# Kernel optimization log

Measured on AMD Instinct MI355X. Metric: run time of the kernel, lower is better.

The kernel has to match this reference:

```python
import jax, jax.numpy as jnp
import numpy as np

NSLICES = 4
HID = 512
IN_FEAT = 342   # input_shape - 1 (last column is phase)
OUT = 311
BATCH = 256


def cubic(y0, y1, y2, y3, mu):
    # Catmull-Rom cubic interpolation, as in the original PFNN code
    return (
        (-0.5 * y0 + 1.5 * y1 - 1.5 * y2 + 0.5 * y3) * mu * mu * mu
        + (y0 - 2.5 * y1 + 2.0 * y2 - 0.5 * y3) * mu * mu
        + (-0.5 * y0 + 0.5 * y2) * mu
        + y1
    )


def setup_inputs() -> dict:
    key = jax.random.key(0)
    ks = jax.random.split(key, 7)
    x = jax.random.uniform(ks[0], (BATCH, IN_FEAT + 1), dtype=jnp.float32)
    s = 0.02
    W0 = jax.random.normal(ks[1], (NSLICES, HID, IN_FEAT), dtype=jnp.float32) * s
    b0 = jax.random.normal(ks[2], (NSLICES, HID), dtype=jnp.float32) * s
    W1 = jax.random.normal(ks[3], (NSLICES, HID, HID), dtype=jnp.float32) * s
    b1 = jax.random.normal(ks[4], (NSLICES, HID), dtype=jnp.float32) * s
    W2 = jax.random.normal(ks[5], (NSLICES, OUT, HID), dtype=jnp.float32) * s
    b2 = jax.random.normal(ks[6], (NSLICES, OUT), dtype=jnp.float32) * s
    return {"x": x, "W0": W0, "b0": b0, "W1": W1, "b1": b1, "W2": W2, "b2": b2}


def reference(x, W0, b0, W1, b1, W2, b2):
    phase = x[:, -1]                       # [B]
    pscale = NSLICES * phase
    mu = jnp.mod(pscale, 1.0)              # [B]
    i1 = jnp.floor(pscale).astype(jnp.int32) % NSLICES
    i0 = (i1 - 1) % NSLICES
    i2 = (i1 + 1) % NSLICES
    i3 = (i1 + 2) % NSLICES
    muW = mu[:, None, None]                # broadcast over (out, in)
    mub = mu[:, None]

    Wb0 = cubic(W0[i0], W0[i1], W0[i2], W0[i3], muW)   # [B, 512, 342]
    bb0 = cubic(b0[i0], b0[i1], b0[i2], b0[i3], mub)   # [B, 512]
    Wb1 = cubic(W1[i0], W1[i1], W1[i2], W1[i3], muW)   # [B, 512, 512]
    bb1 = cubic(b1[i0], b1[i1], b1[i2], b1[i3], mub)
    Wb2 = cubic(W2[i0], W2[i1], W2[i2], W2[i3], muW)   # [B, 311, 512]
    bb2 = cubic(b2[i0], b2[i1], b2[i2], b2[i3], mub)

    h = x[:, :-1]                                       # [B, 342]
    h = jax.nn.elu(jnp.einsum('boi,bi->bo', Wb0, h) + bb0)
    h = jax.nn.elu(jnp.einsum('boi,bi->bo', Wb1, h) + bb1)
    out = jnp.einsum('boi,bi->bo', Wb2, h) + bb2        # [B, 311]
    return out
```

## Files before the change

kernel.cpp:

```cpp
#include <hip/hip_runtime.h>
#include <math.h>

#define HID 512
#define IN_FEAT 342
#define OUTD 311
#define BATCH 256
#define XROW (IN_FEAT + 1)

#define NT1 32
#define NCC1 16
#define NT2 20
#define NCC2 16
#define NCC0 11

typedef unsigned short u16;
typedef short bf16x8 __attribute__((ext_vector_type(8)));
typedef float f32x4 __attribute__((ext_vector_type(4)));

__device__ __forceinline__ u16 f2bf_rne(float v) {
    unsigned int x = __float_as_uint(v);
    unsigned int r = (x + 0x7fffu + ((x >> 16) & 1u)) >> 16;
    return (u16)r;
}
__device__ __forceinline__ float bf2f(u16 u) {
    return __uint_as_float(((unsigned int)u) << 16);
}

union U8 { u16 u[8]; uint4 v; };

__device__ __forceinline__ void split8(const float* __restrict__ src, bf16x8& hi, bf16x8& lo) {
#pragma unroll
    for (int j = 0; j < 8; j++) {
        u16 h = f2bf_rne(src[j]);
        hi[j] = (short)h;
        lo[j] = (short)f2bf_rne(src[j] - bf2f(h));
    }
}

#define NB0 32
#define KLDS0 360
__global__ __launch_bounds__(512, 1) void layer0_fused(
    const float* __restrict__ W0, const float* __restrict__ W1, const float* __restrict__ W2,
    const float* __restrict__ x, const float* __restrict__ bias,
    u16* __restrict__ F1, u16* __restrict__ F2,
    float* __restrict__ Oact, float* __restrict__ H2acc, float* __restrict__ outz)
{
    __shared__ u16 wlds[4 * NCC0 * 1024];
    __shared__ u16 hlds[2 * NB0 * KLDS0];
    __shared__ float accs[4][NB0][17];

    const int blk = (int)blockIdx.x;
    const int bx = (blk >> 3) & 7;
    const int by = (blk & 7) | ((blk >> 6) << 3);
    const int tid = (int)threadIdx.x;
    const int b0 = bx * NB0;
    const int o0 = by * 16;

    for (int idx = tid; idx < 4 * 16 * 44; idx += 512) {
        int s = idx / (16 * 44);
        int rem = idx - s * (16 * 44);
        int rr = rem / 44, c = rem - rr * 44;
        int k = c * 8;
        const float* rp = W0 + (size_t)(s * 512 + o0 + rr) * IN_FEAT;
        float src[8];
        if (k + 8 <= IN_FEAT) {
            const float2* p2 = reinterpret_cast<const float2*>(rp + k);
            float2 v0 = p2[0], v1 = p2[1], v2 = p2[2], v3 = p2[3];
            src[0] = v0.x; src[1] = v0.y; src[2] = v1.x; src[3] = v1.y;
            src[4] = v2.x; src[5] = v2.y; src[6] = v3.x; src[7] = v3.y;
        } else {
#pragma unroll
            for (int j = 0; j < 8; j++) src[j] = (k + j < IN_FEAT) ? rp[k + j] : 0.f;
        }
        U8 hi, lo;
#pragma unroll
        for (int j = 0; j < 8; j++) {
            u16 h = f2bf_rne(src[j]);
            hi.u[j] = h;
            lo.u[j] = f2bf_rne(src[j] - bf2f(h));
        }
        int cc = c >> 2, lane = (c & 3) * 16 + rr;
        *reinterpret_cast<uint4*>(&wlds[(s * NCC0 + cc) * 1024 + lane * 8])       = hi.v;
        *reinterpret_cast<uint4*>(&wlds[(s * NCC0 + cc) * 1024 + 512 + lane * 8]) = lo.v;
    }

    for (int idx = tid; idx < NB0 * 44; idx += 512) {
        int r = idx / 44, c = idx - r * 44;
        int k = c * 8;
        const float* xr = x + (size_t)(b0 + r) * XROW;
        float src[8];
#pragma unroll
        for (int j = 0; j < 8; j++) {
            int kk = k + j;
            src[j] = (kk < IN_FEAT) ? xr[kk] : 0.f;
        }
        bf16x8 hi, lo;
        split8(src, hi, lo);
        *reinterpret_cast<bf16x8*>(&hlds[r * KLDS0 + k])               = hi;
        *reinterpret_cast<bf16x8*>(&hlds[NB0 * KLDS0 + r * KLDS0 + k]) = lo;
    }
    __syncthreads();

    const int lane = tid & 63;
    const int w = tid >> 6;
    const int s = w & 3;
    const int t = w >> 2;
    const int m = lane & 15;
    const int q = lane >> 4;

    const u16* wf  = &wlds[s * NCC0 * 1024 + lane * 8];
    const u16* hp  = &hlds[(t * 16 + m) * KLDS0 + q * 8];
    const u16* hpl = &hlds[NB0 * KLDS0 + (t * 16 + m) * KLDS0 + q * 8];

    const int brow = b0 + t * 16 + m;
    const float ps = 4.f * x[(size_t)brow * XROW + IN_FEAT];
    const float fl = floorf(ps);
    const float mu = ps - fl;
    const int i1 = ((int)fl) & 3;
    const int jj = (s - i1) & 3;
    const float mu2 = mu * mu, mu3 = mu2 * mu;
    const float ds = (jj == 0) ? ( 1.5f * mu3 - 2.5f * mu2 + 1.0f)
                   : (jj == 1) ? (-1.5f * mu3 + 2.0f * mu2 + 0.5f * mu)
                   : (jj == 2) ? ( 0.5f * mu3 - 0.5f * mu2)
                   :             (-0.5f * mu3 + mu2 - 0.5f * mu);

    f32x4 a0 = {0.f, 0.f, 0.f, 0.f};
    f32x4 a1 = {0.f, 0.f, 0.f, 0.f};
    f32x4 a2 = {0.f, 0.f, 0.f, 0.f};
#pragma unroll
    for (int cc = 0; cc < NCC0; ++cc) {
        bf16x8 ah = *reinterpret_cast<const bf16x8*>(wf + cc * 1024);
        bf16x8 al = *reinterpret_cast<const bf16x8*>(wf + cc * 1024 + 512);
        bf16x8 bh = *reinterpret_cast<const bf16x8*>(hp + cc * 32);
        bf16x8 bl = *reinterpret_cast<const bf16x8*>(hpl + cc * 32);
        a0 = __builtin_amdgcn_mfma_f32_16x16x32_bf16(ah, bh, a0, 0, 0, 0);
        a1 = __builtin_amdgcn_mfma_f32_16x16x32_bf16(ah, bl, a1, 0, 0, 0);
        a2 = __builtin_amdgcn_mfma_f32_16x16x32_bf16(al, bh, a2, 0, 0, 0);
    }
    __syncthreads();

    f32x4 sum = a0 + a1 + a2;
#pragma unroll
    for (int r = 0; r < 4; ++r) {
        int o = o0 + q * 4 + r;
        accs[s][t * 16 + m][q * 4 + r] = ds * (sum[r] + bias[(size_t)s * HID + o]);
    }
    __syncthreads();

    const int b_l = tid >> 4;
    const int o_l = tid & 15;
    float vv = accs[0][b_l][o_l] + accs[1][b_l][o_l]
             + accs[2][b_l][o_l] + accs[3][b_l][o_l];
    {
        float e = (vv > 0.f) ? vv : expm1f(vv);
        Oact[(size_t)(b0 + b_l) * HID + o0 + o_l] = e;
    }

    if (blk < 208) {
        const bool w2j = (blk >= 128);
        int l = w2j ? (blk - 128) : blk;
        int js, jot;
        if (w2j) { js = l / 20; jot = l - js * 20; }
        else     { js = l >> 5; jot = l & 31; }
        u16* Fd = w2j ? (F2 + (size_t)(js * NT2 + jot) * NCC2 * 1024)
                      : (F1 + (size_t)(js * NT1 + jot) * NCC1 * 1024);
        for (int idx = tid; idx < 16 * 64; idx += 512) {
            int rr = idx >> 6, c = idx & 63;
            float src[8] = {0.f, 0.f, 0.f, 0.f, 0.f, 0.f, 0.f, 0.f};
            if (!w2j) {
                const float4* p4 = reinterpret_cast<const float4*>(
                    W1 + (size_t)(js * 512 + jot * 16 + rr) * 512 + c * 8);
                float4 v0 = p4[0], v1 = p4[1];
                src[0] = v0.x; src[1] = v0.y; src[2] = v0.z; src[3] = v0.w;
                src[4] = v1.x; src[5] = v1.y; src[6] = v1.z; src[7] = v1.w;
            } else {
                int orow = jot * 16 + rr;
                if (orow < OUTD) {
                    const float4* p4 = reinterpret_cast<const float4*>(
                        W2 + ((size_t)js * OUTD + orow) * 512 + c * 8);
                    float4 v0 = p4[0], v1 = p4[1];
                    src[0] = v0.x; src[1] = v0.y; src[2] = v0.z; src[3] = v0.w;
                    src[4] = v1.x; src[5] = v1.y; src[6] = v1.z; src[7] = v1.w;
                }
            }
            U8 hi, lo;
#pragma unroll
            for (int j = 0; j < 8; j++) {
                u16 h = f2bf_rne(src[j]);
                hi.u[j] = h;
                lo.u[j] = f2bf_rne(src[j] - bf2f(h));
            }
            int cc = c >> 2, jl = (c & 3) * 16 + rr;
            *reinterpret_cast<uint4*>(Fd + cc * 1024 + jl * 8)       = hi.v;
            *reinterpret_cast<uint4*>(Fd + cc * 1024 + 512 + jl * 8) = lo.v;
        }
    } else {
        for (int i = (blk - 208) * 512 + tid; i < 131072 + 79616; i += 48 * 512) {
            if (i < 131072) H2acc[i] = 0.f;
            else            outz[i - 131072] = 0.f;
        }
    }
}

#define KLDS1 264
template<int FINAL, int ACT, int NT, int NBY>
__global__ __launch_bounds__(256, 4) void layer_ks(
    const u16* __restrict__ Wf, const float* __restrict__ x,
    const float* __restrict__ Hin, const float* __restrict__ bias, int Mb,
    float* __restrict__ accout)
{
    union SharedU {
        u16 h[2][16 * KLDS1];
        float acc[4][16][17];
    };
    __shared__ SharedU sm;

    const int blk = (int)blockIdx.x;
    const int bx = (blk >> 3) & 15;
    const int kh = (blk >> 7) & 1;
    const int by = (blk & 7) | ((blk >> 8) << 3);
    if (by >= NBY) return;

    const int tid = (int)threadIdx.x;
    const int b0 = bx * 16;
    const int o0 = by * 16;

    for (int idx = tid; idx < 16 * 32; idx += 256) {
        int r = idx >> 5, c = idx & 31;
        const float4* hv = reinterpret_cast<const float4*>(
            Hin + (size_t)(b0 + r) * HID + kh * 256 + c * 8);
        float4 v0 = hv[0], v1 = hv[1];
        float src[8] = {v0.x, v0.y, v0.z, v0.w, v1.x, v1.y, v1.z, v1.w};
        if (ACT) {
#pragma unroll
            for (int j = 0; j < 8; j++) src[j] = (src[j] > 0.f) ? src[j] : expm1f(src[j]);
        }
        bf16x8 hi, lo;
        split8(src, hi, lo);
        *reinterpret_cast<bf16x8*>(&sm.h[0][r * KLDS1 + c * 8]) = hi;
        *reinterpret_cast<bf16x8*>(&sm.h[1][r * KLDS1 + c * 8]) = lo;
    }
    __syncthreads();

    const int lane = tid & 63;
    const int s = tid >> 6;
    const int m = lane & 15;
    const int q = lane >> 4;

    const u16* wf = Wf + ((size_t)(s * NT + by) * 16 + kh * 8) * 1024 + lane * 8;
    const u16* hp  = &sm.h[0][m * KLDS1 + q * 8];
    const u16* hpl = &sm.h[1][m * KLDS1 + q * 8];

    const int brow = b0 + m;
    const float ps = 4.f * x[(size_t)brow * XROW + IN_FEAT];
    const float fl = floorf(ps);
    const float mu = ps - fl;
    const int i1 = ((int)fl) & 3;
    const int jj = (s - i1) & 3;
    const float mu2 = mu * mu, mu3 = mu2 * mu;
    const float ds = (jj == 0) ? ( 1.5f * mu3 - 2.5f * mu2 + 1.0f)
                   : (jj == 1) ? (-1.5f * mu3 + 2.0f * mu2 + 0.5f * mu)
                   : (jj == 2) ? ( 0.5f * mu3 - 0.5f * mu2)
                   :             (-0.5f * mu3 + mu2 - 0.5f * mu);

    f32x4 a0 = {0.f, 0.f, 0.f, 0.f};
    f32x4 a1 = {0.f, 0.f, 0.f, 0.f};
    f32x4 a2 = {0.f, 0.f, 0.f, 0.f};
#pragma unroll
    for (int cc = 0; cc < 8; ++cc) {
        bf16x8 ah = *reinterpret_cast<const bf16x8*>(wf + cc * 1024);
        bf16x8 al = *reinterpret_cast<const bf16x8*>(wf + cc * 1024 + 512);
        bf16x8 bh = *reinterpret_cast<const bf16x8*>(hp + cc * 32);
        bf16x8 bl = *reinterpret_cast<const bf16x8*>(hpl + cc * 32);
        a0 = __builtin_amdgcn_mfma_f32_16x16x32_bf16(ah, bh, a0, 0, 0, 0);
        a1 = __builtin_amdgcn_mfma_f32_16x16x32_bf16(ah, bl, a1, 0, 0, 0);
        a2 = __builtin_amdgcn_mfma_f32_16x16x32_bf16(al, bh, a2, 0, 0, 0);
    }
    __syncthreads();

    f32x4 sum = a0 + a1 + a2;
#pragma unroll
    for (int r = 0; r < 4; ++r) {
        int o = o0 + q * 4 + r;
        float bb = (kh == 0 && o < Mb) ? bias[(size_t)s * Mb + o] : 0.f;
        sm.acc[s][m][q * 4 + r] = ds * (sum[r] + bb);
    }
    __syncthreads();

    const int b_l = tid >> 4;
    const int o_l = tid & 15;
    float vv = sm.acc[0][b_l][o_l] + sm.acc[1][b_l][o_l]
             + sm.acc[2][b_l][o_l] + sm.acc[3][b_l][o_l];
    const int o = o0 + o_l;
    const int b = b0 + b_l;
    if (FINAL) {
        if (o < OUTD) unsafeAtomicAdd(&accout[(size_t)b * OUTD + o], vv);
    } else {
        unsafeAtomicAdd(&accout[(size_t)b * HID + o], vv);
    }
}

extern "C" void kernel_launch(void* const* d_in, const int* in_sizes, int n_in,
                              void* d_out, int out_size, void* d_ws, size_t ws_size,
                              hipStream_t stream) {
    const float* x  = (const float*)d_in[0];
    const float* W0 = (const float*)d_in[1];
    const float* b0v = (const float*)d_in[2];
    const float* W1 = (const float*)d_in[3];
    const float* b1v = (const float*)d_in[4];
    const float* W2 = (const float*)d_in[5];
    const float* b2v = (const float*)d_in[6];
    float* out = (float*)d_out;

    char* pw = (char*)d_ws;
    auto alloc = [&](size_t bytes) { char* r = pw; pw += (bytes + 255) & ~(size_t)255; return r; };

    u16* F1 = (u16*)alloc((size_t)4 * NT1 * NCC1 * 1024 * 2);
    u16* F2 = (u16*)alloc((size_t)4 * NT2 * NCC2 * 1024 * 2);
    float* H0act = (float*)alloc((size_t)BATCH * HID * 4);
    float* H2acc = (float*)alloc((size_t)BATCH * HID * 4);

    layer0_fused<<<256, 512, 0, stream>>>(
        W0, W1, W2, x, b0v, F1, F2, H0act, H2acc, out);

    layer_ks<0, 0, NT1, 32><<<1024, 256, 0, stream>>>(
        F1, x, H0act, b1v, HID, H2acc);

    layer_ks<1, 1, NT2, 20><<<768, 256, 0, stream>>>(
        F2, x, H2acc, b2v, OUTD, out);
}
```

Baseline: 99.99 us.

## Hoist global weight loads ahead of LDS staging to overlap memory latency

In the fused layer-0 kernel, the W1/W2 reformat job's global loads are now issued at kernel start into registers, before the W0/x staging and the MFMA work, and written out at the end. The staging loops are unrolled with fixed trip counts. In layer_ks, the first four weight fragments are prefetched from global before the activation staging barrier, and the K loop is software-pipelined to load the next fragments while the current ones feed the MFMAs. The aim is to hide global-load latency behind other work, at the cost of more live registers and possible occupancy pressure.

```diff
diff --git a/kernel.cpp b/kernel.cpp
--- a/kernel.cpp
+++ b/kernel.cpp
@@ -56,51 +56,6 @@
     const int b0 = bx * NB0;
     const int o0 = by * 16;
 
-    for (int idx = tid; idx < 4 * 16 * 44; idx += 512) {
-        int s = idx / (16 * 44);
-        int rem = idx - s * (16 * 44);
-        int rr = rem / 44, c = rem - rr * 44;
-        int k = c * 8;
-        const float* rp = W0 + (size_t)(s * 512 + o0 + rr) * IN_FEAT;
-        float src[8];
-        if (k + 8 <= IN_FEAT) {
-            const float2* p2 = reinterpret_cast<const float2*>(rp + k);
-            float2 v0 = p2[0], v1 = p2[1], v2 = p2[2], v3 = p2[3];
-            src[0] = v0.x; src[1] = v0.y; src[2] = v1.x; src[3] = v1.y;
-            src[4] = v2.x; src[5] = v2.y; src[6] = v3.x; src[7] = v3.y;
-        } else {
-#pragma unroll
-            for (int j = 0; j < 8; j++) src[j] = (k + j < IN_FEAT) ? rp[k + j] : 0.f;
-        }
-        U8 hi, lo;
-#pragma unroll
-        for (int j = 0; j < 8; j++) {
-            u16 h = f2bf_rne(src[j]);
-            hi.u[j] = h;
-            lo.u[j] = f2bf_rne(src[j] - bf2f(h));
-        }
-        int cc = c >> 2, lane = (c & 3) * 16 + rr;
-        *reinterpret_cast<uint4*>(&wlds[(s * NCC0 + cc) * 1024 + lane * 8])       = hi.v;
-        *reinterpret_cast<uint4*>(&wlds[(s * NCC0 + cc) * 1024 + 512 + lane * 8]) = lo.v;
-    }
-
-    for (int idx = tid; idx < NB0 * 44; idx += 512) {
-        int r = idx / 44, c = idx - r * 44;
-        int k = c * 8;
-        const float* xr = x + (size_t)(b0 + r) * XROW;
-        float src[8];
-#pragma unroll
-        for (int j = 0; j < 8; j++) {
-            int kk = k + j;
-            src[j] = (kk < IN_FEAT) ? xr[kk] : 0.f;
-        }
-        bf16x8 hi, lo;
-        split8(src, hi, lo);
-        *reinterpret_cast<bf16x8*>(&hlds[r * KLDS0 + k])               = hi;
-        *reinterpret_cast<bf16x8*>(&hlds[NB0 * KLDS0 + r * KLDS0 + k]) = lo;
-    }
-    __syncthreads();
-
     const int lane = tid & 63;
     const int w = tid >> 6;
     const int s = w & 3;
@@ -108,15 +63,107 @@
     const int m = lane & 15;
     const int q = lane >> 4;
 
-    const u16* wf  = &wlds[s * NCC0 * 1024 + lane * 8];
+    const int brow = b0 + t * 16 + m;
+    const float ps = 4.f * x[(size_t)brow * XROW + IN_FEAT];
+
+    const bool sjob = (blk < 208);
+    const bool w2j = sjob && (blk >= 128);
+    int js = 0, jot = 0;
+    u16* Fd = nullptr;
+    float4 sj00 = {0,0,0,0}, sj01 = {0,0,0,0}, sj10 = {0,0,0,0}, sj11 = {0,0,0,0};
+    if (sjob) {
+        int l = w2j ? (blk - 128) : blk;
+        if (w2j) { js = l / 20; jot = l - js * 20; }
+        else     { js = l >> 5; jot = l & 31; }
+        Fd = w2j ? (F2 + (size_t)(js * NT2 + jot) * NCC2 * 1024)
+                 : (F1 + (size_t)(js * NT1 + jot) * NCC1 * 1024);
+        {
+            int rr = tid >> 6, c = tid & 63;
+            if (!w2j) {
+                const float4* p4 = reinterpret_cast<const float4*>(
+                    W1 + (size_t)(js * 512 + jot * 16 + rr) * 512 + c * 8);
+                sj00 = p4[0]; sj01 = p4[1];
+            } else if (jot * 16 + rr < OUTD) {
+                const float4* p4 = reinterpret_cast<const float4*>(
+                    W2 + ((size_t)js * OUTD + jot * 16 + rr) * 512 + c * 8);
+                sj00 = p4[0]; sj01 = p4[1];
+            }
+        }
+        {
+            int idx = tid + 512;
+            int rr = idx >> 6, c = idx & 63;
+            if (!w2j) {
+                const float4* p4 = reinterpret_cast<const float4*>(
+                    W1 + (size_t)(js * 512 + jot * 16 + rr) * 512 + c * 8);
+                sj10 = p4[0]; sj11 = p4[1];
+            } else if (jot * 16 + rr < OUTD) {
+                const float4* p4 = reinterpret_cast<const float4*>(
+                    W2 + ((size_t)js * OUTD + jot * 16 + rr) * 512 + c * 8);
+                sj10 = p4[0]; sj11 = p4[1];
+            }
+        }
+    }
+
+#pragma unroll
+    for (int r6 = 0; r6 < 6; ++r6) {
+        int idx = tid + r6 * 512;
+        if (idx < 4 * 16 * 44) {
+            int ss = idx / (16 * 44);
+            int rem = idx - ss * (16 * 44);
+            int rr = rem / 44, c = rem - rr * 44;
+            int k = c * 8;
+            const float* rp = W0 + (size_t)(ss * 512 + o0 + rr) * IN_FEAT;
+            float src[8];
+            if (k + 8 <= IN_FEAT) {
+                const float2* p2 = reinterpret_cast<const float2*>(rp + k);
+                float2 v0 = p2[0], v1 = p2[1], v2 = p2[2], v3 = p2[3];
+                src[0] = v0.x; src[1] = v0.y; src[2] = v1.x; src[3] = v1.y;
+                src[4] = v2.x; src[5] = v2.y; src[6] = v3.x; src[7] = v3.y;
+            } else {
+#pragma unroll
+                for (int j = 0; j < 8; j++) src[j] = (k + j < IN_FEAT) ? rp[k + j] : 0.f;
+            }
+            U8 hi, lo;
+#pragma unroll
+            for (int j = 0; j < 8; j++) {
+                u16 h = f2bf_rne(src[j]);
+                hi.u[j] = h;
+                lo.u[j] = f2bf_rne(src[j] - bf2f(h));
+            }
+            int cc = c >> 2, fl = (c & 3) * 16 + rr;
+            *reinterpret_cast<uint4*>(&wlds[(ss * NCC0 + cc) * 1024 + fl * 8])       = hi.v;
+            *reinterpret_cast<uint4*>(&wlds[(ss * NCC0 + cc) * 1024 + 512 + fl * 8]) = lo.v;
+        }
+    }
+
+#pragma unroll
+    for (int r3 = 0; r3 < 3; ++r3) {
+        int idx = tid + r3 * 512;
+        if (idx < NB0 * 44) {
+            int r = idx / 44, c = idx - r * 44;
+            int k = c * 8;
+            const float* xr = x + (size_t)(b0 + r) * XROW;
+            float src[8];
+#pragma unroll
+            for (int j = 0; j < 8; j++) {
+                int kk = k + j;
+                src[j] = (kk < IN_FEAT) ? xr[kk] : 0.f;
+            }
+            bf16x8 hi, lo;
+            split8(src, hi, lo);
+            *reinterpret_cast<bf16x8*>(&hlds[r * KLDS0 + k])               = hi;
+            *reinterpret_cast<bf16x8*>(&hlds[NB0 * KLDS0 + r * KLDS0 + k]) = lo;
+        }
+    }
+    __syncthreads();
+
+    const u16* wfl = &wlds[s * NCC0 * 1024 + lane * 8];
     const u16* hp  = &hlds[(t * 16 + m) * KLDS0 + q * 8];
     const u16* hpl = &hlds[NB0 * KLDS0 + (t * 16 + m) * KLDS0 + q * 8];
 
-    const int brow = b0 + t * 16 + m;
-    const float ps = 4.f * x[(size_t)brow * XROW + IN_FEAT];
-    const float fl = floorf(ps);
-    const float mu = ps - fl;
-    const int i1 = ((int)fl) & 3;
+    const float fl2 = floorf(ps);
+    const float mu = ps - fl2;
+    const int i1 = ((int)fl2) & 3;
     const int jj = (s - i1) & 3;
     const float mu2 = mu * mu, mu3 = mu2 * mu;
     const float ds = (jj == 0) ? ( 1.5f * mu3 - 2.5f * mu2 + 1.0f)
@@ -129,8 +176,8 @@
     f32x4 a2 = {0.f, 0.f, 0.f, 0.f};
 #pragma unroll
     for (int cc = 0; cc < NCC0; ++cc) {
-        bf16x8 ah = *reinterpret_cast<const bf16x8*>(wf + cc * 1024);
-        bf16x8 al = *reinterpret_cast<const bf16x8*>(wf + cc * 1024 + 512);
+        bf16x8 ah = *reinterpret_cast<const bf16x8*>(wfl + cc * 1024);
+        bf16x8 al = *reinterpret_cast<const bf16x8*>(wfl + cc * 1024 + 512);
         bf16x8 bh = *reinterpret_cast<const bf16x8*>(hp + cc * 32);
         bf16x8 bl = *reinterpret_cast<const bf16x8*>(hpl + cc * 32);
         a0 = __builtin_amdgcn_mfma_f32_16x16x32_bf16(ah, bh, a0, 0, 0, 0);
@@ -156,33 +203,9 @@
         Oact[(size_t)(b0 + b_l) * HID + o0 + o_l] = e;
     }
 
-    if (blk < 208) {
-        const bool w2j = (blk >= 128);
-        int l = w2j ? (blk - 128) : blk;
-        int js, jot;
-        if (w2j) { js = l / 20; jot = l - js * 20; }
-        else     { js = l >> 5; jot = l & 31; }
-        u16* Fd = w2j ? (F2 + (size_t)(js * NT2 + jot) * NCC2 * 1024)
-                      : (F1 + (size_t)(js * NT1 + jot) * NCC1 * 1024);
-        for (int idx = tid; idx < 16 * 64; idx += 512) {
-            int rr = idx >> 6, c = idx & 63;
-            float src[8] = {0.f, 0.f, 0.f, 0.f, 0.f, 0.f, 0.f, 0.f};
-            if (!w2j) {
-                const float4* p4 = reinterpret_cast<const float4*>(
-                    W1 + (size_t)(js * 512 + jot * 16 + rr) * 512 + c * 8);
-                float4 v0 = p4[0], v1 = p4[1];
-                src[0] = v0.x; src[1] = v0.y; src[2] = v0.z; src[3] = v0.w;
-                src[4] = v1.x; src[5] = v1.y; src[6] = v1.z; src[7] = v1.w;
-            } else {
-                int orow = jot * 16 + rr;
-                if (orow < OUTD) {
-                    const float4* p4 = reinterpret_cast<const float4*>(
-                        W2 + ((size_t)js * OUTD + orow) * 512 + c * 8);
-                    float4 v0 = p4[0], v1 = p4[1];
-                    src[0] = v0.x; src[1] = v0.y; src[2] = v0.z; src[3] = v0.w;
-                    src[4] = v1.x; src[5] = v1.y; src[6] = v1.z; src[7] = v1.w;
-                }
-            }
+    if (sjob) {
+        auto put = [&](int idx, float4 va, float4 vb) {
+            float src[8] = {va.x, va.y, va.z, va.w, vb.x, vb.y, vb.z, vb.w};
             U8 hi, lo;
 #pragma unroll
             for (int j = 0; j < 8; j++) {
@@ -190,11 +213,14 @@
                 hi.u[j] = h;
                 lo.u[j] = f2bf_rne(src[j] - bf2f(h));
             }
+            int rr = idx >> 6, c = idx & 63;
             int cc = c >> 2, jl = (c & 3) * 16 + rr;
             *reinterpret_cast<uint4*>(Fd + cc * 1024 + jl * 8)       = hi.v;
             *reinterpret_cast<uint4*>(Fd + cc * 1024 + 512 + jl * 8) = lo.v;
-        }
-    } else {
+        };
+        put(tid, sj00, sj01);
+        put(tid + 512, sj10, sj11);
+    } else if (blk >= 208) {
         for (int i = (blk - 208) * 512 + tid; i < 131072 + 79616; i += 48 * 512) {
             if (i < 131072) H2acc[i] = 0.f;
             else            outz[i - 131072] = 0.f;
@@ -203,6 +229,15 @@
 }
 
 #define KLDS1 264
+#define KSTEP(CC, WH, WL, PF, PFCC)                                              \
+    { bf16x8 bh = *reinterpret_cast<const bf16x8*>(hp + (CC) * 32);              \
+      bf16x8 bl = *reinterpret_cast<const bf16x8*>(hpl + (CC) * 32);             \
+      a0 = __builtin_amdgcn_mfma_f32_16x16x32_bf16(WH, bh, a0, 0, 0, 0);         \
+      a1 = __builtin_amdgcn_mfma_f32_16x16x32_bf16(WH, bl, a1, 0, 0, 0);         \
+      a2 = __builtin_amdgcn_mfma_f32_16x16x32_bf16(WL, bh, a2, 0, 0, 0);         \
+      if (PF) { WH = *reinterpret_cast<const bf16x8*>(wf + (PFCC) * 1024);       \
+                WL = *reinterpret_cast<const bf16x8*>(wf + (PFCC) * 1024 + 512); } }
+
 template<int FINAL, int ACT, int NT, int NBY>
 __global__ __launch_bounds__(256, 4) void layer_ks(
     const u16* __restrict__ Wf, const float* __restrict__ x,
@@ -224,8 +259,27 @@
     const int tid = (int)threadIdx.x;
     const int b0 = bx * 16;
     const int o0 = by * 16;
-
-    for (int idx = tid; idx < 16 * 32; idx += 256) {
+    const int lane = tid & 63;
+    const int s = tid >> 6;
+    const int m = lane & 15;
+    const int q = lane >> 4;
+
+    const int brow = b0 + m;
+    const float ps = 4.f * x[(size_t)brow * XROW + IN_FEAT];
+
+    const u16* wf = Wf + ((size_t)(s * NT + by) * 16 + kh * 8) * 1024 + lane * 8;
+    bf16x8 wh0 = *reinterpret_cast<const bf16x8*>(wf);
+    bf16x8 wl0 = *reinterpret_cast<const bf16x8*>(wf + 512);
+    bf16x8 wh1 = *reinterpret_cast<const bf16x8*>(wf + 1024);
+    bf16x8 wl1 = *reinterpret_cast<const bf16x8*>(wf + 1024 + 512);
+    bf16x8 wh2 = *reinterpret_cast<const bf16x8*>(wf + 2048);
+    bf16x8 wl2 = *reinterpret_cast<const bf16x8*>(wf + 2048 + 512);
+    bf16x8 wh3 = *reinterpret_cast<const bf16x8*>(wf + 3072);
+    bf16x8 wl3 = *reinterpret_cast<const bf16x8*>(wf + 3072 + 512);
+
+#pragma unroll
+    for (int r2 = 0; r2 < 2; ++r2) {
+        int idx = tid + r2 * 256;
         int r = idx >> 5, c = idx & 31;
         const float4* hv = reinterpret_cast<const float4*>(
             Hin + (size_t)(b0 + r) * HID + kh * 256 + c * 8);
@@ -242,17 +296,9 @@
     }
     __syncthreads();
 
-    const int lane = tid & 63;
-    const int s = tid >> 6;
-    const int m = lane & 15;
-    const int q = lane >> 4;
-
-    const u16* wf = Wf + ((size_t)(s * NT + by) * 16 + kh * 8) * 1024 + lane * 8;
     const u16* hp  = &sm.h[0][m * KLDS1 + q * 8];
     const u16* hpl = &sm.h[1][m * KLDS1 + q * 8];
 
-    const int brow = b0 + m;
-    const float ps = 4.f * x[(size_t)brow * XROW + IN_FEAT];
     const float fl = floorf(ps);
     const float mu = ps - fl;
     const int i1 = ((int)fl) & 3;
@@ -266,16 +312,14 @@
     f32x4 a0 = {0.f, 0.f, 0.f, 0.f};
     f32x4 a1 = {0.f, 0.f, 0.f, 0.f};
     f32x4 a2 = {0.f, 0.f, 0.f, 0.f};
-#pragma unroll
-    for (int cc = 0; cc < 8; ++cc) {
-        bf16x8 ah = *reinterpret_cast<const bf16x8*>(wf + cc * 1024);
-        bf16x8 al = *reinterpret_cast<const bf16x8*>(wf + cc * 1024 + 512);
-        bf16x8 bh = *reinterpret_cast<const bf16x8*>(hp + cc * 32);
-        bf16x8 bl = *reinterpret_cast<const bf16x8*>(hpl + cc * 32);
-        a0 = __builtin_amdgcn_mfma_f32_16x16x32_bf16(ah, bh, a0, 0, 0, 0);
-        a1 = __builtin_amdgcn_mfma_f32_16x16x32_bf16(ah, bl, a1, 0, 0, 0);
-        a2 = __builtin_amdgcn_mfma_f32_16x16x32_bf16(al, bh, a2, 0, 0, 0);
-    }
+    KSTEP(0, wh0, wl0, 1, 4)
+    KSTEP(1, wh1, wl1, 1, 5)
+    KSTEP(2, wh2, wl2, 1, 6)
+    KSTEP(3, wh3, wl3, 1, 7)
+    KSTEP(4, wh0, wl0, 0, 0)
+    KSTEP(5, wh1, wl1, 0, 0)
+    KSTEP(6, wh2, wl2, 0, 0)
+    KSTEP(7, wh3, wl3, 0, 0)
     __syncthreads();
 
     f32x4 sum = a0 + a1 + a2;
```

Measured after the change: 99.38 us. Within noise of the previous version (-0.6%).
